# Optimization experiments

Hardware: AMD Instinct MI355X
Metric: run time of the kernel (lower is better)

Reference implementation:

```python
import jax, jax.numpy as jnp
import numpy as np

B, T, C, H, NUM_EDGE_TYPES = 2, 512, 256, 8, 16


def setup_inputs() -> dict:
    key = jax.random.key(0)
    ks = jax.random.split(key, 8)
    init = 0.02
    x = jax.random.normal(ks[0], (B, T, C), dtype=jnp.float32)
    bias_matrix = jax.random.randint(ks[1], (B, T, T), 0, NUM_EDGE_TYPES)
    w_attn = jax.random.normal(ks[2], (C, 3 * C), dtype=jnp.float32) * init
    w_proj = jax.random.normal(ks[3], (C, C), dtype=jnp.float32) * init
    w_edge_k = jax.random.normal(ks[4], (C, C), dtype=jnp.float32) * init
    w_edge_v = jax.random.normal(ks[5], (C, C), dtype=jnp.float32) * init
    edge_emb_table = jax.random.normal(ks[6], (NUM_EDGE_TYPES, C), dtype=jnp.float32)
    attn_bias_table = jax.random.normal(ks[7], (NUM_EDGE_TYPES, H), dtype=jnp.float32)
    return {
        "x": x,
        "bias_matrix": bias_matrix,
        "w_attn": w_attn,
        "w_proj": w_proj,
        "w_edge_k": w_edge_k,
        "w_edge_v": w_edge_v,
        "edge_emb_table": edge_emb_table,
        "attn_bias_table": attn_bias_table,
    }


def reference(x, bias_matrix, w_attn, w_proj, w_edge_k, w_edge_v,
              edge_emb_table, attn_bias_table):
    b, t, c = x.shape
    h = attn_bias_table.shape[1]
    e = c // h
    scale = jnp.sqrt(jnp.asarray(e, x.dtype))

    qkv = x @ w_attn                              # (B,T,3C)
    q, k, v = jnp.split(qkv, 3, axis=-1)
    # (B,H,T,E)
    q = q.reshape(b, t, h, e).transpose(0, 2, 1, 3)
    k = k.reshape(b, t, h, e).transpose(0, 2, 1, 3)
    v = v.reshape(b, t, h, e).transpose(0, 2, 1, 3)

    # edge-type embeddings and per-pair k/v modulation, (B,T,T,H,E)
    ee = edge_emb_table[bias_matrix]              # (B,T,T,C)
    e_k = (ee @ w_edge_k).reshape(b, t, t, h, e)
    e_v = (ee @ w_edge_v).reshape(b, t, t, h, e)

    # scores[b,h,i,j] = sum_e q[b,h,i,e] * k[b,h,j,e] * e_k[b, j, i, h, e]
    # (torch: e_k permuted to (B,H,j,i,E), broadcast-multiplied by k then
    #  contracted with q via 'bhie,bhjie->bhij')
    scores = jnp.einsum('bhie,bhje,bjihe->bhij', q, k, e_k) / scale

    causal = jnp.tril(jnp.ones((t, t), dtype=bool))  # (T,T)
    scores = jnp.where(causal, scores, -jnp.inf)

    # edge-type attention bias: (B,T,T,H) -> (B,H,T,T), zeroed above diagonal
    bias = attn_bias_table[bias_matrix].transpose(0, 3, 1, 2)
    bias = jnp.where(causal, bias, jnp.zeros((), bias.dtype))

    attn = jax.nn.softmax(scores + bias, axis=-1)  # (B,H,T,T)

    # y[b,h,i,e] = sum_j attn[b,h,i,j] * v[b,h,j,e] * e_v[b, j, i, h, e]
    y = jnp.einsum('bhij,bhje,bjihe->bhie', attn, v, e_v)
    y = y.transpose(0, 2, 1, 3).reshape(b, t, c)
    return y @ w_proj
```

## Files before the change

kernel.cpp:

```cpp
#include <hip/hip_runtime.h>
#include <hip/hip_bf16.h>
#include <math.h>

#define Bdim 2
#define Tdim 512
#define Cdim 256
#define Hdim 8
#define Edim 32
#define NTYPES 16
#define TI 8
#define JT 128

__global__ __launch_bounds__(256) void pre_kernel(
    const float* __restrict__ A, const float* __restrict__ Bw,
    const float* __restrict__ emb, const float* __restrict__ wk,
    const float* __restrict__ wv,
    float* __restrict__ qT, float* __restrict__ kT, float* __restrict__ vT,
    float* __restrict__ ekt, float* __restrict__ evt)
{
    __shared__ float smem[16 * 34 + 16 * 64];
    int tid = threadIdx.x;

    if (blockIdx.x >= 384) {
        int t = blockIdx.x - 384;
        float* se = smem;
        se[tid] = emb[t * Cdim + tid];
        __syncthreads();
        float a = 0.f, b = 0.f;
        for (int k = 0; k < Cdim; ++k) {
            float ev = se[k];
            a = fmaf(ev, wk[k * Cdim + tid], a);
            b = fmaf(ev, wv[k * Cdim + tid], b);
        }
        ekt[t * Cdim + tid] = a;
        evt[t * Cdim + tid] = b;
        return;
    }

    const int N = 3 * Cdim;
    const int K = Cdim;
    float (*As)[34] = (float(*)[34])smem;
    float (*Bs)[64] = (float(*)[64])(smem + 16 * 34);
    int m0 = (blockIdx.x / 12) * 32;
    int n0 = (blockIdx.x % 12) * 64;
    int tr = tid >> 4, tc = tid & 15;
    float acc[2][4] = {};
    int bkr = tid >> 4, bcq = (tid & 15) * 4;

    for (int k0 = 0; k0 < K; k0 += 16) {
        if (tid < 128) {
            int r = tid >> 2, kq = (tid & 3) * 4;
            float4 av = *(const float4*)(A + (size_t)(m0 + r) * K + k0 + kq);
            As[kq + 0][r] = av.x;
            As[kq + 1][r] = av.y;
            As[kq + 2][r] = av.z;
            As[kq + 3][r] = av.w;
        }
        float4 bv = *(const float4*)(Bw + (size_t)(k0 + bkr) * N + n0 + bcq);
        *(float4*)&Bs[bkr][bcq] = bv;
        __syncthreads();
#pragma unroll
        for (int kk = 0; kk < 16; ++kk) {
            float2 a2 = *(float2*)&As[kk][tr * 2];
            float4 b4 = *(float4*)&Bs[kk][tc * 4];
            acc[0][0] = fmaf(a2.x, b4.x, acc[0][0]);
            acc[0][1] = fmaf(a2.x, b4.y, acc[0][1]);
            acc[0][2] = fmaf(a2.x, b4.z, acc[0][2]);
            acc[0][3] = fmaf(a2.x, b4.w, acc[0][3]);
            acc[1][0] = fmaf(a2.y, b4.x, acc[1][0]);
            acc[1][1] = fmaf(a2.y, b4.y, acc[1][1]);
            acc[1][2] = fmaf(a2.y, b4.z, acc[1][2]);
            acc[1][3] = fmaf(a2.y, b4.w, acc[1][3]);
        }
        __syncthreads();
    }
    int sec = n0 >> 8;
    float* dst = (sec == 0) ? qT : (sec == 1) ? kT : vT;
    int cc0 = (n0 & 255) + tc * 4;
    int h = cc0 >> 5;
    int e0 = cc0 & 31;
#pragma unroll
    for (int i = 0; i < 2; ++i) {
        int m = m0 + tr * 2 + i;
        int bq = m >> 9, t = m & (Tdim - 1);
        float4 val = make_float4(acc[i][0], acc[i][1], acc[i][2], acc[i][3]);
        *(float4*)&dst[(((size_t)bq * Hdim + h) * Tdim + t) * Edim + e0] = val;
    }
}

__global__ __launch_bounds__(512, 4) void attn_kernel(
    const float* __restrict__ qT, const float* __restrict__ kT,
    const float* __restrict__ vT, const int* __restrict__ bm,
    const float* __restrict__ ekt, const float* __restrict__ evt,
    const float* __restrict__ abt, float* __restrict__ y)
{
    __shared__ float kv[2][JT][32];
    __shared__ float qm[TI][NTYPES][36];
    __shared__ float ss[TI][516];
    __shared__ unsigned int st1pf[Tdim];
    __shared__ unsigned int st2pf[Tdim];
    __shared__ float sekt[NTYPES][36];
    __shared__ float sevt[NTYPES][36];
    __shared__ float sq[TI][36];
    __shared__ float sabt[NTYPES];
    __shared__ float sinv[TI];

    float* spart = (float*)qm;

    const int pairIdx = blockIdx.x;
    const int bh = blockIdx.y;
    const int h = bh & (Hdim - 1);
    const int b = bh >> 3;
    const int tid = threadIdx.x;
    const int wave = tid >> 6;
    const int lane = tid & 63;
    const float inv_scale = 0.17677669529663687f;

    const float* qbase = qT + (size_t)bh * Tdim * Edim;
    const float* kbase = kT + (size_t)bh * Tdim * Edim;
    const float* vbase = vT + (size_t)bh * Tdim * Edim;
    const int* bmb = bm + (size_t)b * Tdim * Tdim;

    const int sr0 = tid >> 3;
    const int seq4 = (tid & 7) << 2;
    const int ssw = seq4 ^ ((sr0 & 7) << 2);

    if (tid < 128) {
        int t = tid >> 3, eq = tid & 7;
        *(float4*)&sekt[t][eq * 4] = *(const float4*)&ekt[t * Cdim + h * Edim + eq * 4];
        *(float4*)&sevt[t][eq * 4] = *(const float4*)&evt[t * Cdim + h * Edim + eq * 4];
    }
    if (tid < NTYPES) sabt[tid] = abt[tid * Hdim + h];

    for (int rep = 0; rep < 2; ++rep) {
        int tau = rep ? (63 - pairIdx) : pairIdx;
        int i0 = tau * TI;
        int imax = i0 + TI - 1;
        int njt = (imax >> 7) + 1;
        int jmax = njt << 7;

        __syncthreads();

        if (tid < TI * 8) {
            int r = tid >> 3, eq = tid & 7;
            *(float4*)&sq[r][eq * 4] =
                *(const float4*)&qbase[(size_t)(i0 + r) * Edim + eq * 4];
        }
        if (tid < jmax) {
            const int* rowp = bmb + (size_t)tid * Tdim + i0;
            int4 lo = *(const int4*)rowp;
            int4 hi = *(const int4*)(rowp + 4);
            st1pf[tid] =
                ((unsigned)(lo.x & 15)) | (((unsigned)(lo.y & 15)) << 4) |
                (((unsigned)(lo.z & 15)) << 8) | (((unsigned)(lo.w & 15)) << 12) |
                (((unsigned)(hi.x & 15)) << 16) | (((unsigned)(hi.y & 15)) << 20) |
                (((unsigned)(hi.z & 15)) << 24) | (((unsigned)(hi.w & 15)) << 28);
            unsigned w2 = 0;
#pragma unroll
            for (int iiq = 0; iiq < 8; ++iiq)
                w2 |= ((unsigned)(bmb[(size_t)(i0 + iiq) * Tdim + tid] & 15)) << (iiq * 4);
            st2pf[tid] = w2;
        }
        *(float4*)&kv[0][sr0][ssw] =
            *(const float4*)&kbase[((size_t)sr0 << 5) + seq4];
        *(float4*)&kv[0][sr0 + 64][ssw] =
            *(const float4*)&kbase[(((size_t)sr0 + 64) << 5) + seq4];
        __syncthreads();
        for (int idx = tid; idx < TI * NTYPES * 8; idx += 512) {
            int eq = idx & 7;
            int t = (idx >> 3) & (NTYPES - 1);
            int r = idx >> 7;
            float4 qv = *(float4*)&sq[r][eq * 4];
            float4 ev = *(float4*)&sekt[t][eq * 4];
            float4 o;
            o.x = qv.x * ev.x; o.y = qv.y * ev.y;
            o.z = qv.z * ev.z; o.w = qv.w * ev.w;
            *(float4*)&qm[r][t][eq * 4] = o;
        }
        __syncthreads();

        int cur = 0;
        for (int jt = 0; jt < njt; ++jt) {
            int j0 = jt << 7;
            const bool pf = (jt + 1) < njt;
            float4 n0, n1;
            if (pf) {
                const float* src = kbase + ((size_t)(j0 + 128) << 5);
                n0 = *(const float4*)(src + ((size_t)sr0 << 5) + seq4);
                n1 = *(const float4*)(src + (((size_t)sr0 + 64) << 5) + seq4);
            }

            int jsub = wave & 1;
            int jl = (jsub << 6) + lane;
            int j = j0 + jl;
            const int xsw = (jl & 7) << 2;
            float4 k4[8];
#pragma unroll
            for (int eq = 0; eq < 8; ++eq)
                k4[eq] = *(float4*)&kv[cur][jl][(eq << 2) ^ xsw];
            unsigned tp = st1pf[j];
            unsigned tp2 = st2pf[j];

#pragma unroll
            for (int u = 0; u < 2; ++u) {
                int ii = (wave >> 1) + (u << 2);
                int i = i0 + ii;
                if (j0 + (jsub << 6) > i) continue;
                int t1 = (tp >> (ii * 4)) & 15;
                int t2 = (tp2 >> (ii * 4)) & 15;
                float s = 0.f;
#pragma unroll
                for (int eq = 0; eq < 8; ++eq) {
                    float4 qv = *(float4*)&qm[ii][t1][eq * 4];
                    s = fmaf(qv.x, k4[eq].x, s);
                    s = fmaf(qv.y, k4[eq].y, s);
                    s = fmaf(qv.z, k4[eq].z, s);
                    s = fmaf(qv.w, k4[eq].w, s);
                }
                if (j <= i) ss[ii][j] = s * inv_scale + sabt[t2];
            }

            if (pf) {
                *(float4*)&kv[cur ^ 1][sr0][ssw] = n0;
                *(float4*)&kv[cur ^ 1][sr0 + 64][ssw] = n1;
            }
            __syncthreads();
            cur ^= 1;
        }

        *(float4*)&kv[0][sr0][ssw] =
            *(const float4*)&vbase[((size_t)sr0 << 5) + seq4];
        *(float4*)&kv[0][sr0 + 64][ssw] =
            *(const float4*)&vbase[(((size_t)sr0 + 64) << 5) + seq4];

        {
            int ii = wave;
            int i = i0 + ii;
            float m = -1e30f;
            for (int j = lane; j <= i; j += 64) m = fmaxf(m, ss[ii][j]);
            for (int off = 32; off; off >>= 1) m = fmaxf(m, __shfl_xor(m, off));
            float sum = 0.f;
            for (int j = lane; j <= i; j += 64) {
                float p = __expf(ss[ii][j] - m);
                ss[ii][j] = p;
                sum += p;
            }
            for (int off = 32; off; off >>= 1) sum += __shfl_xor(sum, off);
            if (lane == 0) sinv[ii] = 1.0f / sum;
        }
        __syncthreads();

        float4 acc[TI];
#pragma unroll
        for (int ii = 0; ii < TI; ++ii) acc[ii] = make_float4(0.f, 0.f, 0.f, 0.f);
        int gid = tid >> 3;
        int eqg4 = (tid & 7) << 2;
        cur = 0;
        for (int jt = 0; jt < njt; ++jt) {
            int j0 = jt << 7;
            const bool pf = (jt + 1) < njt;
            float4 n0, n1;
            if (pf) {
                const float* src = vbase + ((size_t)(j0 + 128) << 5);
                n0 = *(const float4*)(src + ((size_t)sr0 << 5) + seq4);
                n1 = *(const float4*)(src + (((size_t)sr0 + 64) << 5) + seq4);
            }
#pragma unroll
            for (int sub = 0; sub < 2; ++sub) {
                int jl = (sub << 6) + gid;
                int j = j0 + jl;
                float4 v4 = *(float4*)&kv[cur][jl][eqg4 ^ ((jl & 7) << 2)];
                unsigned tp = st1pf[j];
#pragma unroll
                for (int ii = 0; ii < TI; ++ii) {
                    int i = i0 + ii;
                    if (j0 + (sub << 6) > i) continue;
                    float p = (j <= i) ? ss[ii][j] : 0.f;
                    int t1 = (tp >> (ii * 4)) & 15;
                    float4 ev = *(float4*)&sevt[t1][eqg4];
                    acc[ii].x = fmaf(p * ev.x, v4.x, acc[ii].x);
                    acc[ii].y = fmaf(p * ev.y, v4.y, acc[ii].y);
                    acc[ii].z = fmaf(p * ev.z, v4.z, acc[ii].z);
                    acc[ii].w = fmaf(p * ev.w, v4.w, acc[ii].w);
                }
            }
            if (pf) {
                *(float4*)&kv[cur ^ 1][sr0][ssw] = n0;
                *(float4*)&kv[cur ^ 1][sr0 + 64][ssw] = n1;
            }
            __syncthreads();
            cur ^= 1;
        }
#pragma unroll
        for (int ii = 0; ii < TI; ++ii) {
#pragma unroll
            for (int m = 8; m <= 32; m <<= 1) {
                acc[ii].x += __shfl_xor(acc[ii].x, m);
                acc[ii].y += __shfl_xor(acc[ii].y, m);
                acc[ii].z += __shfl_xor(acc[ii].z, m);
                acc[ii].w += __shfl_xor(acc[ii].w, m);
            }
        }
        if (lane < 8) {
#pragma unroll
            for (int ii = 0; ii < TI; ++ii)
                *(float4*)&spart[((wave * TI + ii) << 5) + lane * 4] = acc[ii];
        }
        __syncthreads();
        if (tid < TI * Edim) {
            int ii = tid >> 5, e = tid & 31;
            float yv = 0.f;
#pragma unroll
            for (int w = 0; w < 8; ++w) yv += spart[((w * TI + ii) << 5) + e];
            yv *= sinv[ii];
            y[((size_t)(b * Tdim + i0 + ii)) * Cdim + h * Edim + e] = yv;
        }
    }
}

__global__ __launch_bounds__(256) void proj_gemm_kernel(
    const float* __restrict__ A, const float* __restrict__ Bw,
    float* __restrict__ out)
{
    const int N = Cdim;
    const int K = Cdim;
    __shared__ float As[16][34];
    __shared__ float Bs[16][64];
    int m0 = blockIdx.y * 32;
    int n0 = blockIdx.x * 64;
    int tid = threadIdx.x;
    int tr = tid >> 4, tc = tid & 15;
    float acc[2][4] = {};
    int bkr = tid >> 4, bcq = (tid & 15) * 4;

    for (int k0 = 0; k0 < K; k0 += 16) {
        if (tid < 128) {
            int r = tid >> 2, kq = (tid & 3) * 4;
            float4 av = *(const float4*)(A + (size_t)(m0 + r) * K + k0 + kq);
            As[kq + 0][r] = av.x;
            As[kq + 1][r] = av.y;
            As[kq + 2][r] = av.z;
            As[kq + 3][r] = av.w;
        }
        float4 bv = *(const float4*)(Bw + (size_t)(k0 + bkr) * N + n0 + bcq);
        *(float4*)&Bs[bkr][bcq] = bv;
        __syncthreads();
#pragma unroll
        for (int kk = 0; kk < 16; ++kk) {
            float2 a2 = *(float2*)&As[kk][tr * 2];
            float4 b4 = *(float4*)&Bs[kk][tc * 4];
            acc[0][0] = fmaf(a2.x, b4.x, acc[0][0]);
            acc[0][1] = fmaf(a2.x, b4.y, acc[0][1]);
            acc[0][2] = fmaf(a2.x, b4.z, acc[0][2]);
            acc[0][3] = fmaf(a2.x, b4.w, acc[0][3]);
            acc[1][0] = fmaf(a2.y, b4.x, acc[1][0]);
            acc[1][1] = fmaf(a2.y, b4.y, acc[1][1]);
            acc[1][2] = fmaf(a2.y, b4.z, acc[1][2]);
            acc[1][3] = fmaf(a2.y, b4.w, acc[1][3]);
        }
        __syncthreads();
    }
#pragma unroll
    for (int i = 0; i < 2; ++i) {
        int m = m0 + tr * 2 + i;
        float4 val = make_float4(acc[i][0], acc[i][1], acc[i][2], acc[i][3]);
        *(float4*)&out[(size_t)m * N + n0 + tc * 4] = val;
    }
}

extern "C" void kernel_launch(void* const* d_in, const int* in_sizes, int n_in,
                              void* d_out, int out_size, void* d_ws, size_t ws_size,
                              hipStream_t stream) {
    (void)in_sizes; (void)n_in; (void)out_size; (void)ws_size;
    const float* x = (const float*)d_in[0];
    const int* bias_matrix = (const int*)d_in[1];
    const float* w_attn = (const float*)d_in[2];
    const float* w_proj = (const float*)d_in[3];
    const float* w_edge_k = (const float*)d_in[4];
    const float* w_edge_v = (const float*)d_in[5];
    const float* edge_emb = (const float*)d_in[6];
    const float* attn_bias = (const float*)d_in[7];
    float* out = (float*)d_out;

    const size_t n_qkv = (size_t)Bdim * Hdim * Tdim * Edim;
    float* ws = (float*)d_ws;
    float* qT = ws;
    float* kT = qT + n_qkv;
    float* vT = kT + n_qkv;
    float* y = vT + n_qkv;
    float* ekt = y + (size_t)Bdim * Tdim * Cdim;
    float* evt = ekt + (size_t)NTYPES * Cdim;

    pre_kernel<<<400, 256, 0, stream>>>(x, w_attn, edge_emb, w_edge_k, w_edge_v,
                                        qT, kT, vT, ekt, evt);
    attn_kernel<<<dim3(32, 16), 512, 0, stream>>>(qT, kT, vT, bias_matrix,
                                                  ekt, evt, attn_bias, y);
    proj_gemm_kernel<<<dim3(4, 32), 256, 0, stream>>>(y, w_proj, out);
}
```

Measured before the change: 135.3 us.

## Shrink attention LDS footprint and launch one block per query tile for occupancy

The attention kernel drops the paired-tile loop and launches one block per 8-row query tile, ordering blocks from longest to shortest causal range. The K/V shared buffer goes from double to single buffered, and the precomputed q*edge_k table is removed; the triple product is now computed inline from sq and sekt. spart reuses the score buffer. Together with launch bounds raised to 6 blocks per SM, this cuts LDS use to allow more resident blocks, at the cost of extra multiplies in the score loop, an added barrier per tile, and less overlap of global loads with compute.

```diff
diff --git a/kernel.cpp b/kernel.cpp
--- a/kernel.cpp
+++ b/kernel.cpp
@@ -88,14 +88,13 @@
     }
 }
 
-__global__ __launch_bounds__(512, 4) void attn_kernel(
+__global__ __launch_bounds__(512, 6) void attn_kernel(
     const float* __restrict__ qT, const float* __restrict__ kT,
     const float* __restrict__ vT, const int* __restrict__ bm,
     const float* __restrict__ ekt, const float* __restrict__ evt,
     const float* __restrict__ abt, float* __restrict__ y)
 {
-    __shared__ float kv[2][JT][32];
-    __shared__ float qm[TI][NTYPES][36];
+    __shared__ float kv[JT][32];
     __shared__ float ss[TI][516];
     __shared__ unsigned int st1pf[Tdim];
     __shared__ unsigned int st2pf[Tdim];
@@ -105,10 +104,10 @@
     __shared__ float sabt[NTYPES];
     __shared__ float sinv[TI];
 
-    float* spart = (float*)qm;
-
-    const int pairIdx = blockIdx.x;
-    const int bh = blockIdx.y;
+    float* spart = (float*)ss;
+
+    const int tau = 63 - (blockIdx.x >> 4);
+    const int bh = blockIdx.x & 15;
     const int h = bh & (Hdim - 1);
     const int b = bh >> 3;
     const int tid = threadIdx.x;
@@ -125,196 +124,165 @@
     const int seq4 = (tid & 7) << 2;
     const int ssw = seq4 ^ ((sr0 & 7) << 2);
 
+    const int i0 = tau * TI;
+    const int imax = i0 + TI - 1;
+    const int njt = (imax >> 7) + 1;
+    const int jmax = njt << 7;
+
     if (tid < 128) {
         int t = tid >> 3, eq = tid & 7;
         *(float4*)&sekt[t][eq * 4] = *(const float4*)&ekt[t * Cdim + h * Edim + eq * 4];
         *(float4*)&sevt[t][eq * 4] = *(const float4*)&evt[t * Cdim + h * Edim + eq * 4];
     }
     if (tid < NTYPES) sabt[tid] = abt[tid * Hdim + h];
-
-    for (int rep = 0; rep < 2; ++rep) {
-        int tau = rep ? (63 - pairIdx) : pairIdx;
-        int i0 = tau * TI;
-        int imax = i0 + TI - 1;
-        int njt = (imax >> 7) + 1;
-        int jmax = njt << 7;
-
-        __syncthreads();
-
-        if (tid < TI * 8) {
-            int r = tid >> 3, eq = tid & 7;
-            *(float4*)&sq[r][eq * 4] =
-                *(const float4*)&qbase[(size_t)(i0 + r) * Edim + eq * 4];
-        }
-        if (tid < jmax) {
-            const int* rowp = bmb + (size_t)tid * Tdim + i0;
-            int4 lo = *(const int4*)rowp;
-            int4 hi = *(const int4*)(rowp + 4);
-            st1pf[tid] =
-                ((unsigned)(lo.x & 15)) | (((unsigned)(lo.y & 15)) << 4) |
-                (((unsigned)(lo.z & 15)) << 8) | (((unsigned)(lo.w & 15)) << 12) |
-                (((unsigned)(hi.x & 15)) << 16) | (((unsigned)(hi.y & 15)) << 20) |
-                (((unsigned)(hi.z & 15)) << 24) | (((unsigned)(hi.w & 15)) << 28);
-            unsigned w2 = 0;
-#pragma unroll
-            for (int iiq = 0; iiq < 8; ++iiq)
-                w2 |= ((unsigned)(bmb[(size_t)(i0 + iiq) * Tdim + tid] & 15)) << (iiq * 4);
-            st2pf[tid] = w2;
-        }
-        *(float4*)&kv[0][sr0][ssw] =
-            *(const float4*)&kbase[((size_t)sr0 << 5) + seq4];
-        *(float4*)&kv[0][sr0 + 64][ssw] =
-            *(const float4*)&kbase[(((size_t)sr0 + 64) << 5) + seq4];
-        __syncthreads();
-        for (int idx = tid; idx < TI * NTYPES * 8; idx += 512) {
-            int eq = idx & 7;
-            int t = (idx >> 3) & (NTYPES - 1);
-            int r = idx >> 7;
-            float4 qv = *(float4*)&sq[r][eq * 4];
-            float4 ev = *(float4*)&sekt[t][eq * 4];
-            float4 o;
-            o.x = qv.x * ev.x; o.y = qv.y * ev.y;
-            o.z = qv.z * ev.z; o.w = qv.w * ev.w;
-            *(float4*)&qm[r][t][eq * 4] = o;
-        }
-        __syncthreads();
-
-        int cur = 0;
-        for (int jt = 0; jt < njt; ++jt) {
-            int j0 = jt << 7;
-            const bool pf = (jt + 1) < njt;
-            float4 n0, n1;
-            if (pf) {
-                const float* src = kbase + ((size_t)(j0 + 128) << 5);
-                n0 = *(const float4*)(src + ((size_t)sr0 << 5) + seq4);
-                n1 = *(const float4*)(src + (((size_t)sr0 + 64) << 5) + seq4);
+    if (tid < TI * 8) {
+        int r = tid >> 3, eq = tid & 7;
+        *(float4*)&sq[r][eq * 4] =
+            *(const float4*)&qbase[(size_t)(i0 + r) * Edim + eq * 4];
+    }
+    if (tid < jmax) {
+        const int* rowp = bmb + (size_t)tid * Tdim + i0;
+        int4 lo = *(const int4*)rowp;
+        int4 hi = *(const int4*)(rowp + 4);
+        st1pf[tid] =
+            ((unsigned)(lo.x & 15)) | (((unsigned)(lo.y & 15)) << 4) |
+            (((unsigned)(lo.z & 15)) << 8) | (((unsigned)(lo.w & 15)) << 12) |
+            (((unsigned)(hi.x & 15)) << 16) | (((unsigned)(hi.y & 15)) << 20) |
+            (((unsigned)(hi.z & 15)) << 24) | (((unsigned)(hi.w & 15)) << 28);
+        unsigned w2 = 0;
+#pragma unroll
+        for (int iiq = 0; iiq < 8; ++iiq)
+            w2 |= ((unsigned)(bmb[(size_t)(i0 + iiq) * Tdim + tid] & 15)) << (iiq * 4);
+        st2pf[tid] = w2;
+    }
+    *(float4*)&kv[sr0][ssw] = *(const float4*)&kbase[((size_t)sr0 << 5) + seq4];
+    *(float4*)&kv[sr0 + 64][ssw] =
+        *(const float4*)&kbase[(((size_t)sr0 + 64) << 5) + seq4];
+    __syncthreads();
+
+    for (int jt = 0; jt < njt; ++jt) {
+        int j0 = jt << 7;
+        const float* nsrc =
+            (jt + 1 < njt) ? (kbase + ((size_t)(j0 + 128) << 5)) : vbase;
+        float4 n0 = *(const float4*)(nsrc + ((size_t)sr0 << 5) + seq4);
+        float4 n1 = *(const float4*)(nsrc + (((size_t)sr0 + 64) << 5) + seq4);
+
+        int jsub = wave & 1;
+        int jl = (jsub << 6) + lane;
+        int j = j0 + jl;
+        const int xsw = (jl & 7) << 2;
+        float4 k4[8];
+#pragma unroll
+        for (int eq = 0; eq < 8; ++eq)
+            k4[eq] = *(float4*)&kv[jl][(eq << 2) ^ xsw];
+        unsigned tp = st1pf[j];
+        unsigned tp2 = st2pf[j];
+
+#pragma unroll
+        for (int u = 0; u < 2; ++u) {
+            int ii = (wave >> 1) + (u << 2);
+            int i = i0 + ii;
+            if (j0 + (jsub << 6) > i) continue;
+            int t1 = (tp >> (ii * 4)) & 15;
+            int t2 = (tp2 >> (ii * 4)) & 15;
+            float s0 = 0.f, s1 = 0.f;
+#pragma unroll
+            for (int eq = 0; eq < 8; ++eq) {
+                float4 qv = *(float4*)&sq[ii][eq * 4];
+                float4 ee = *(float4*)&sekt[t1][eq * 4];
+                s0 = fmaf(qv.x * k4[eq].x, ee.x, s0);
+                s1 = fmaf(qv.y * k4[eq].y, ee.y, s1);
+                s0 = fmaf(qv.z * k4[eq].z, ee.z, s0);
+                s1 = fmaf(qv.w * k4[eq].w, ee.w, s1);
             }
-
-            int jsub = wave & 1;
-            int jl = (jsub << 6) + lane;
+            if (j <= i) ss[ii][j] = (s0 + s1) * inv_scale + sabt[t2];
+        }
+        __syncthreads();
+        *(float4*)&kv[sr0][ssw] = n0;
+        *(float4*)&kv[sr0 + 64][ssw] = n1;
+        if (jt + 1 < njt) __syncthreads();
+    }
+
+    {
+        int ii = wave;
+        int i = i0 + ii;
+        float m = -1e30f;
+        for (int j = lane; j <= i; j += 64) m = fmaxf(m, ss[ii][j]);
+        for (int off = 32; off; off >>= 1) m = fmaxf(m, __shfl_xor(m, off));
+        float sum = 0.f;
+        for (int j = lane; j <= i; j += 64) {
+            float p = __expf(ss[ii][j] - m);
+            ss[ii][j] = p;
+            sum += p;
+        }
+        for (int off = 32; off; off >>= 1) sum += __shfl_xor(sum, off);
+        if (lane == 0) sinv[ii] = 1.0f / sum;
+    }
+    __syncthreads();
+
+    float4 acc[TI];
+#pragma unroll
+    for (int ii = 0; ii < TI; ++ii) acc[ii] = make_float4(0.f, 0.f, 0.f, 0.f);
+    int gid = tid >> 3;
+    int eqg4 = (tid & 7) << 2;
+    for (int jt = 0; jt < njt; ++jt) {
+        int j0 = jt << 7;
+        const bool pf = (jt + 1) < njt;
+        float4 n0, n1;
+        if (pf) {
+            const float* nsrc = vbase + ((size_t)(j0 + 128) << 5);
+            n0 = *(const float4*)(nsrc + ((size_t)sr0 << 5) + seq4);
+            n1 = *(const float4*)(nsrc + (((size_t)sr0 + 64) << 5) + seq4);
+        }
+#pragma unroll
+        for (int sub = 0; sub < 2; ++sub) {
+            int jl = (sub << 6) + gid;
             int j = j0 + jl;
-            const int xsw = (jl & 7) << 2;
-            float4 k4[8];
-#pragma unroll
-            for (int eq = 0; eq < 8; ++eq)
-                k4[eq] = *(float4*)&kv[cur][jl][(eq << 2) ^ xsw];
+            float4 v4 = *(float4*)&kv[jl][eqg4 ^ ((jl & 7) << 2)];
             unsigned tp = st1pf[j];
-            unsigned tp2 = st2pf[j];
-
-#pragma unroll
-            for (int u = 0; u < 2; ++u) {
-                int ii = (wave >> 1) + (u << 2);
+#pragma unroll
+            for (int ii = 0; ii < TI; ++ii) {
                 int i = i0 + ii;
-                if (j0 + (jsub << 6) > i) continue;
+                if (j0 + (sub << 6) > i) continue;
+                float p = (j <= i) ? ss[ii][j] : 0.f;
                 int t1 = (tp >> (ii * 4)) & 15;
-                int t2 = (tp2 >> (ii * 4)) & 15;
-                float s = 0.f;
-#pragma unroll
-                for (int eq = 0; eq < 8; ++eq) {
-                    float4 qv = *(float4*)&qm[ii][t1][eq * 4];
-                    s = fmaf(qv.x, k4[eq].x, s);
-                    s = fmaf(qv.y, k4[eq].y, s);
-                    s = fmaf(qv.z, k4[eq].z, s);
-                    s = fmaf(qv.w, k4[eq].w, s);
-                }
-                if (j <= i) ss[ii][j] = s * inv_scale + sabt[t2];
+                float4 ev = *(float4*)&sevt[t1][eqg4];
+                acc[ii].x = fmaf(p * ev.x, v4.x, acc[ii].x);
+                acc[ii].y = fmaf(p * ev.y, v4.y, acc[ii].y);
+                acc[ii].z = fmaf(p * ev.z, v4.z, acc[ii].z);
+                acc[ii].w = fmaf(p * ev.w, v4.w, acc[ii].w);
             }
-
-            if (pf) {
-                *(float4*)&kv[cur ^ 1][sr0][ssw] = n0;
-                *(float4*)&kv[cur ^ 1][sr0 + 64][ssw] = n1;
-            }
+        }
+        __syncthreads();
+        if (pf) {
+            *(float4*)&kv[sr0][ssw] = n0;
+            *(float4*)&kv[sr0 + 64][ssw] = n1;
             __syncthreads();
-            cur ^= 1;
-        }
-
-        *(float4*)&kv[0][sr0][ssw] =
-            *(const float4*)&vbase[((size_t)sr0 << 5) + seq4];
-        *(float4*)&kv[0][sr0 + 64][ssw] =
-            *(const float4*)&vbase[(((size_t)sr0 + 64) << 5) + seq4];
-
-        {
-            int ii = wave;
-            int i = i0 + ii;
-            float m = -1e30f;
-            for (int j = lane; j <= i; j += 64) m = fmaxf(m, ss[ii][j]);
-            for (int off = 32; off; off >>= 1) m = fmaxf(m, __shfl_xor(m, off));
-            float sum = 0.f;
-            for (int j = lane; j <= i; j += 64) {
-                float p = __expf(ss[ii][j] - m);
-                ss[ii][j] = p;
-                sum += p;
-            }
-            for (int off = 32; off; off >>= 1) sum += __shfl_xor(sum, off);
-            if (lane == 0) sinv[ii] = 1.0f / sum;
-        }
-        __syncthreads();
-
-        float4 acc[TI];
-#pragma unroll
-        for (int ii = 0; ii < TI; ++ii) acc[ii] = make_float4(0.f, 0.f, 0.f, 0.f);
-        int gid = tid >> 3;
-        int eqg4 = (tid & 7) << 2;
-        cur = 0;
-        for (int jt = 0; jt < njt; ++jt) {
-            int j0 = jt << 7;
-            const bool pf = (jt + 1) < njt;
-            float4 n0, n1;
-            if (pf) {
-                const float* src = vbase + ((size_t)(j0 + 128) << 5);
-                n0 = *(const float4*)(src + ((size_t)sr0 << 5) + seq4);
-                n1 = *(const float4*)(src + (((size_t)sr0 + 64) << 5) + seq4);
-            }
-#pragma unroll
-            for (int sub = 0; sub < 2; ++sub) {
-                int jl = (sub << 6) + gid;
-                int j = j0 + jl;
-                float4 v4 = *(float4*)&kv[cur][jl][eqg4 ^ ((jl & 7) << 2)];
-                unsigned tp = st1pf[j];
-#pragma unroll
-                for (int ii = 0; ii < TI; ++ii) {
-                    int i = i0 + ii;
-                    if (j0 + (sub << 6) > i) continue;
-                    float p = (j <= i) ? ss[ii][j] : 0.f;
-                    int t1 = (tp >> (ii * 4)) & 15;
-                    float4 ev = *(float4*)&sevt[t1][eqg4];
-                    acc[ii].x = fmaf(p * ev.x, v4.x, acc[ii].x);
-                    acc[ii].y = fmaf(p * ev.y, v4.y, acc[ii].y);
-                    acc[ii].z = fmaf(p * ev.z, v4.z, acc[ii].z);
-                    acc[ii].w = fmaf(p * ev.w, v4.w, acc[ii].w);
-                }
-            }
-            if (pf) {
-                *(float4*)&kv[cur ^ 1][sr0][ssw] = n0;
-                *(float4*)&kv[cur ^ 1][sr0 + 64][ssw] = n1;
-            }
-            __syncthreads();
-            cur ^= 1;
-        }
-#pragma unroll
-        for (int ii = 0; ii < TI; ++ii) {
-#pragma unroll
-            for (int m = 8; m <= 32; m <<= 1) {
-                acc[ii].x += __shfl_xor(acc[ii].x, m);
-                acc[ii].y += __shfl_xor(acc[ii].y, m);
-                acc[ii].z += __shfl_xor(acc[ii].z, m);
-                acc[ii].w += __shfl_xor(acc[ii].w, m);
-            }
-        }
-        if (lane < 8) {
-#pragma unroll
-            for (int ii = 0; ii < TI; ++ii)
-                *(float4*)&spart[((wave * TI + ii) << 5) + lane * 4] = acc[ii];
-        }
-        __syncthreads();
-        if (tid < TI * Edim) {
-            int ii = tid >> 5, e = tid & 31;
-            float yv = 0.f;
-#pragma unroll
-            for (int w = 0; w < 8; ++w) yv += spart[((w * TI + ii) << 5) + e];
-            yv *= sinv[ii];
-            y[((size_t)(b * Tdim + i0 + ii)) * Cdim + h * Edim + e] = yv;
-        }
+        }
+    }
+#pragma unroll
+    for (int ii = 0; ii < TI; ++ii) {
+#pragma unroll
+        for (int m = 8; m <= 32; m <<= 1) {
+            acc[ii].x += __shfl_xor(acc[ii].x, m);
+            acc[ii].y += __shfl_xor(acc[ii].y, m);
+            acc[ii].z += __shfl_xor(acc[ii].z, m);
+            acc[ii].w += __shfl_xor(acc[ii].w, m);
+        }
+    }
+    if (lane < 8) {
+#pragma unroll
+        for (int ii = 0; ii < TI; ++ii)
+            *(float4*)&spart[((wave * TI + ii) << 5) + lane * 4] = acc[ii];
+    }
+    __syncthreads();
+    if (tid < TI * Edim) {
+        int ii = tid >> 5, e = tid & 31;
+        float yv = 0.f;
+#pragma unroll
+        for (int w = 0; w < 8; ++w) yv += spart[((w * TI + ii) << 5) + e];
+        yv *= sinv[ii];
+        y[((size_t)(b * Tdim + i0 + ii)) * Cdim + h * Edim + e] = yv;
     }
 }
 
@@ -393,7 +361,7 @@
 
     pre_kernel<<<400, 256, 0, stream>>>(x, w_attn, edge_emb, w_edge_k, w_edge_v,
                                         qT, kT, vT, ekt, evt);
-    attn_kernel<<<dim3(32, 16), 512, 0, stream>>>(qT, kT, vT, bias_matrix,
-                                                  ekt, evt, attn_bias, y);
+    attn_kernel<<<dim3(64 * 16), 512, 0, stream>>>(qT, kT, vT, bias_matrix,
+                                                   ekt, evt, attn_bias, y);
     proj_gemm_kernel<<<dim3(4, 32), 256, 0, stream>>>(y, w_proj, out);
 }
```

After: 165.3 us. +22.2%, slower.
